# Optimization experiments

Hardware: AMD Instinct MI355X
Metric: run time of the kernel (lower is better)

The kernel has to match this reference:

```python
import jax, jax.numpy as jnp
import numpy as np
from jax import lax

BN_INV = float(1.0 / np.sqrt(1.0 + 1e-5))  # BatchNorm eval: running_mean=0, running_var=1


def _block(x, w, b, g, beta, stride):
    # Conv3x3(stride, pad=1) -> BN(eval) -> ReLU -> MaxPool2
    x = lax.conv_general_dilated(x, w, (stride, stride), [(1, 1), (1, 1)],
                                 dimension_numbers=('NCHW', 'OIHW', 'NCHW'))
    x = x + b[None, :, None, None]
    x = x * (g * BN_INV)[None, :, None, None] + beta[None, :, None, None]
    x = jax.nn.relu(x)
    return lax.reduce_window(x, -jnp.inf, lax.max, (1, 1, 2, 2), (1, 1, 2, 2), 'VALID')


def _gru(x, wi, wh, bi, bh):
    # torch-style GRU, batch_first. x: (B, T, D)
    B = x.shape[0]
    H = wh.shape[1]

    def step(h, xt):
        gi = xt @ wi.T + bi
        gh = h @ wh.T + bh
        ir, iz, inn = jnp.split(gi, 3, axis=1)
        hr, hz, hn = jnp.split(gh, 3, axis=1)
        r = jax.nn.sigmoid(ir + hr)
        z = jax.nn.sigmoid(iz + hz)
        nn_ = jnp.tanh(inn + r * hn)
        h2 = (1.0 - z) * nn_ + z * h
        return h2, h2

    h0 = jnp.zeros((B, H), x.dtype)
    _, ys = lax.scan(step, h0, jnp.swapaxes(x, 0, 1))
    return jnp.swapaxes(ys, 0, 1)  # (B, T, H)


def setup_inputs() -> dict:
    key = jax.random.key(0)
    ks = jax.random.split(key, 32)
    rn = lambda i, shape, s: jax.random.normal(ks[i], shape, jnp.float32) * s
    inp = {
        'support': rn(0, (5, 5, 1, 224, 224), 1.0),
        'query': rn(1, (15, 1, 224, 224), 1.0),
        'conv_w1': rn(2, (32, 1, 3, 3), 0.3), 'conv_b1': rn(3, (32,), 0.1),
        'conv_w2': rn(4, (64, 32, 3, 3), 0.06), 'conv_b2': rn(5, (64,), 0.1),
        'conv_w3': rn(6, (128, 64, 3, 3), 0.04), 'conv_b3': rn(7, (128,), 0.1),
        'conv_w4': rn(8, (256, 128, 3, 3), 0.03), 'conv_b4': rn(9, (256,), 0.1),
        'bn_g1': 1.0 + rn(10, (32,), 0.05), 'bn_be1': rn(11, (32,), 0.05),
        'bn_g2': 1.0 + rn(12, (64,), 0.05), 'bn_be2': rn(13, (64,), 0.05),
        'bn_g3': 1.0 + rn(14, (128,), 0.05), 'bn_be3': rn(15, (128,), 0.05),
        'bn_g4': 1.0 + rn(16, (256,), 0.05), 'bn_be4': rn(17, (256,), 0.05),
        'att_w': rn(18, (64, 256), 0.06), 'att_b': rn(19, (64,), 0.05),
        'gru_wi0': rn(20, (384, 512), 0.04), 'gru_wh0': rn(21, (384, 128), 0.08),
        'gru_bi0': rn(22, (384,), 0.05), 'gru_bh0': rn(23, (384,), 0.05),
        'gru_wi1': rn(24, (384, 128), 0.08), 'gru_wh1': rn(25, (384, 128), 0.08),
        'gru_bi1': rn(26, (384,), 0.05), 'gru_bh1': rn(27, (384,), 0.05),
        'trans_w': rn(28, (1, 128), 0.08), 'trans_b': rn(29, (1,), 0.05),
    }
    return inp


def reference(support, query, conv_w1, conv_b1, conv_w2, conv_b2, conv_w3, conv_b3,
              conv_w4, conv_b4, bn_g1, bn_be1, bn_g2, bn_be2, bn_g3, bn_be3,
              bn_g4, bn_be4, att_w, att_b, gru_wi0, gru_wh0, gru_bi0, gru_bh0,
              gru_wi1, gru_wh1, gru_bi1, gru_bh1, trans_w, trans_b):
    n, k, c, w = support.shape[0], support.shape[1], support.shape[2], support.shape[3]
    qk = query.shape[0]

    def enc(x):
        x = _block(x, conv_w1, conv_b1, bn_g1, bn_be1, 2)
        x = _block(x, conv_w2, conv_b2, bn_g2, bn_be2, 1)
        x = _block(x, conv_w3, conv_b3, bn_g3, bn_be3, 1)
        x = _block(x, conv_w4, conv_b4, bn_g4, bn_be4, 1)
        B, F_, H_, W_ = x.shape
        return x.reshape(B, F_, H_ * W_).transpose(0, 2, 1)  # (B, seq, feat)

    hf = enc(support.reshape(n * k, c, w, w))  # (nk, S, f)
    qf = enc(query)                            # (qk, T, f)

    # ItemQueryAttention: score[q,s,t,u] = sum_h tanh(W(q_t) * W(h_u))
    Wq = qf @ att_w.T + att_b  # (qk, T, h)
    Wh = hf @ att_w.T + att_b  # (nk, S, h)
    scores = jnp.tanh(Wq[:, None, :, None, :] * Wh[None, :, None, :, :]).sum(-1)  # (qk,nk,T,S)
    att = jax.nn.softmax(scores, axis=3)
    attended = jnp.einsum('qsTS,sSf->qsTf', att, hf)  # (qk, nk, T, f)

    T_, f = qf.shape[1], qf.shape[2]
    qrep = jnp.broadcast_to(qf[:, None], (qk, n * k, T_, f))
    x = jnp.concatenate([attended, qrep], axis=-1).reshape(qk * n * k, T_, 2 * f)

    h = _gru(x, gru_wi0, gru_wh0, gru_bi0, gru_bh0)
    h = _gru(h, gru_wi1, gru_wh1, gru_bi1, gru_bh1)

    logits = (h[:, -1, :] @ trans_w.T + trans_b).reshape(qk, n, k).sum(axis=2)  # (qk, n)
    return jax.nn.log_softmax(logits, axis=1)
```

## Files before the change

### kernel.cpp

```cpp
#include <hip/hip_runtime.h>
#include <hip/hip_bf16.h>
#include <math.h>

typedef unsigned short u16;
typedef unsigned int u32;
typedef __attribute__((ext_vector_type(8))) short bf16x8v;
typedef __attribute__((ext_vector_type(4))) float f32x4;

constexpr int NS = 25, NQ = 15, NB = 40;
constexpr int B3 = 375;
constexpr int T49 = 49;
constexpr float BN_INV = 0.9999950000374997f;

constexpr size_t A1_OFF    = 0;
constexpr size_t X2_OFF    = 16056320;
constexpr size_t P2_OFF    = 48168960;
constexpr size_t X3_OFF    = 0;
constexpr size_t P3_OFF    = 56197120;
constexpr size_t X4_OFF    = 16056320;
constexpr size_t FEATT_OFF = 60211200;
constexpr size_t PROJ_OFF  = 24084480;
constexpr size_t ATT_OFF   = 24586240;
constexpr size_t GI_OFF    = 62218240;
constexpr size_t Y0_OFF    = 0;
constexpr size_t HFIN_OFF  = 90442240;
constexpr size_t WBH_OFF   = 91027456;
constexpr size_t WBL_OFF   = 92325888;
constexpr size_t W2_E = 0;
constexpr size_t W3_E = 18432;
constexpr size_t W4_E = 92160;
constexpr size_t AW_E = 387072;
constexpr size_t WI0_E = 403456;
constexpr size_t WI1_E = 600064;

static __device__ __forceinline__ u16 f2b(float f) {
  __hip_bfloat16 h = __float2bfloat16(f);
  return *reinterpret_cast<u16*>(&h);
}
static __device__ __forceinline__ float b2f(u16 u) {
  return __uint_as_float((u32)u << 16);
}
static __device__ __forceinline__ void split8(const float* v, u32* hp, u32* lp) {
  u16 h[8], l[8];
#pragma unroll
  for (int j = 0; j < 8; ++j) {
    const u16 hb = f2b(v[j]);
    h[j] = hb;
    l[j] = f2b(v[j] - b2f(hb));
  }
#pragma unroll
  for (int j = 0; j < 4; ++j) {
    hp[j] = (u32)h[2 * j] | ((u32)h[2 * j + 1] << 16);
    lp[j] = (u32)l[2 * j] | ((u32)l[2 * j + 1] << 16);
  }
}
constexpr float LOG2E = 1.4426950408889634f;
static __device__ __forceinline__ float fsigmoid(float x) {
  return __builtin_amdgcn_rcpf(1.f + __builtin_amdgcn_exp2f(-x * LOG2E));
}
static __device__ __forceinline__ float ftanh(float x) {
  return 1.f - 2.f * __builtin_amdgcn_rcpf(__builtin_amdgcn_exp2f(x * (2.f * LOG2E)) + 1.f);
}

__global__ void cvt_split(const float* __restrict__ x, u16* __restrict__ oh,
                          u16* __restrict__ ol, int n) {
  int i = blockIdx.x * 256 + threadIdx.x;
  if (i >= n) return;
  const float v = x[i];
  const u16 h = f2b(v);
  oh[i] = h;
  ol[i] = f2b(v - b2f(h));
}
__global__ void cvt_conv_w_split(const float* __restrict__ w, u16* __restrict__ oh,
                                 u16* __restrict__ ol, int OC, int IC) {
  const int n = OC * IC * 9;
  int i = blockIdx.x * 256 + threadIdx.x;
  if (i >= n) return;
  const int oc = i / (IC * 9), rem = i % (IC * 9);
  const int e = rem / IC, ic = rem % IC;
  const int ky = e / 3, kx = e % 3;
  const float v = w[((size_t)(oc * IC + ic) * 3 + ky) * 3 + kx];
  const u16 h = f2b(v);
  oh[i] = h;
  ol[i] = f2b(v - b2f(h));
}

__global__ __launch_bounds__(256) void conv1_pool(
    const float* __restrict__ support, const float* __restrict__ query,
    const float* __restrict__ w1, const float* __restrict__ cb1,
    const float* __restrict__ g1, const float* __restrict__ be1,
    float* __restrict__ out) {
  __shared__ float wl[288], scl[32], shl[32], cbl[32];
  const int tid = threadIdx.x;
  for (int l = tid; l < 288; l += 256) wl[l] = w1[l];
  if (tid < 32) { scl[tid] = g1[tid] * BN_INV; shl[tid] = be1[tid]; cbl[tid] = cb1[tid]; }
  __syncthreads();
  const int oc = tid & 31;
  const int p = blockIdx.x * 8 + (tid >> 5);
  const int ox = p % 56, oy = (p / 56) % 56, b = p / 3136;
  const float* in_b = (b < NS) ? (support + (size_t)b * 50176)
                               : (query + (size_t)(b - NS) * 50176);
  const int iy0 = 4 * oy - 1, ix0 = 4 * ox - 1;
  float pat[5][5];
#pragma unroll
  for (int dy = 0; dy < 5; ++dy) {
    const int iy = iy0 + dy;
#pragma unroll
    for (int dx = 0; dx < 5; ++dx) {
      const int ix = ix0 + dx;
      pat[dy][dx] = (iy >= 0 && iy < 224 && ix >= 0 && ix < 224)
                        ? in_b[(size_t)iy * 224 + ix] : 0.f;
    }
  }
  const float* wp = &wl[oc * 9];
  float mx = 0.f;
#pragma unroll
  for (int py = 0; py < 2; ++py)
#pragma unroll
    for (int px = 0; px < 2; ++px) {
      float acc = 0.f;
#pragma unroll
      for (int ky = 0; ky < 3; ++ky)
#pragma unroll
        for (int kx = 0; kx < 3; ++kx)
          acc += pat[2 * py + ky][2 * px + kx] * wp[ky * 3 + kx];
      float v = (acc + cbl[oc]) * scl[oc] + shl[oc];
      mx = fmaxf(mx, v);
    }
  out[(size_t)p * 32 + oc] = mx;
}

__global__ void maxpool2_f32(const float* __restrict__ X, float* __restrict__ Y,
                             int Bn, int H, int W, int C) {
  const int OH = H >> 1, OW = W >> 1;
  const int cpr = C >> 2;
  const int chunks = Bn * OH * OW * cpr;
  for (int i = blockIdx.x * blockDim.x + threadIdx.x; i < chunks;
       i += gridDim.x * blockDim.x) {
    const int c4 = i % cpr, m = i / cpr;
    const int ox = m % OW, oy = (m / OW) % OH, b = m / (OW * OH);
    const size_t base = (((size_t)b * H + 2 * oy) * W + 2 * ox) * C + (c4 << 2);
    const float4 r0 = *(const float4*)&X[base];
    const float4 r1 = *(const float4*)&X[base + C];
    const float4 r2 = *(const float4*)&X[base + (size_t)W * C];
    const float4 r3 = *(const float4*)&X[base + (size_t)W * C + C];
    float4 o;
    o.x = fmaxf(fmaxf(r0.x, r1.x), fmaxf(r2.x, r3.x));
    o.y = fmaxf(fmaxf(r0.y, r1.y), fmaxf(r2.y, r3.y));
    o.z = fmaxf(fmaxf(r0.z, r1.z), fmaxf(r2.z, r3.z));
    o.w = fmaxf(fmaxf(r0.w, r1.w), fmaxf(r2.w, r3.w));
    *(float4*)&Y[(size_t)m * C + (c4 << 2)] = o;
  }
}

template <int AMODE, int EPI>
__global__ __launch_bounds__(256) void sgemm(
    const float* __restrict__ A, const float* __restrict__ A2, int M, int K,
    const u16* __restrict__ Bh, const u16* __restrict__ Bl,
    const float* __restrict__ p0, const float* __restrict__ p1,
    const float* __restrict__ p2, float* __restrict__ Cout, int ldc,
    int H, int W, int IC, int icb) {
  __shared__ u16 Ash[64][72], Asl[64][72];
  __shared__ u16 Bsh[64][72], Bsl[64][72];
  const int tid = threadIdx.x;
  const int lane = tid & 63, wv = tid >> 6;
  const int wy = wv >> 1, wx = wv & 1;
  const int n0 = blockIdx.x * 64, m0 = blockIdx.y * 64;
  f32x4 acc[2][2] = {{{0, 0, 0, 0}, {0, 0, 0, 0}}, {{0, 0, 0, 0}, {0, 0, 0, 0}}};
  for (int k0 = 0; k0 < K; k0 += 64) {
#pragma unroll
    for (int s = 0; s < 2; ++s) {
      const int c = s * 256 + tid;
      const int row = c >> 3, kc = (c & 7) << 3;
      const int gm = m0 + row, gk = k0 + kc;
      float4 x0 = {0, 0, 0, 0}, x1 = {0, 0, 0, 0};
      if (AMODE == 0) {
        if (gm < M && gk < K) {
          const float* p = A + (size_t)gm * K + gk;
          x0 = *(const float4*)p; x1 = *(const float4*)(p + 4);
        }
      } else if (AMODE == 1) {
        if (gm < M) {
          const float* p;
          if (gk < 256) {
            p = A + (size_t)gm * 256 + gk;
          } else {
            const int b = gm / T49, t = gm % T49, q = b / NS;
            p = A2 + (((size_t)(NS + q) * T49 + t) << 8) + (gk - 256);
          }
          x0 = *(const float4*)p; x1 = *(const float4*)(p + 4);
        }
      } else {
        if (gm < M && gk < K) {
          const int ox = gm % W, t_ = gm / W;
          const int oy = t_ % H, b = t_ / H;
          const int e = gk >> icb, ic = gk & (IC - 1);
          const int ky = e / 3, kx = e - 3 * (e / 3);
          const int iy = oy + ky - 1, ix = ox + kx - 1;
          if (iy >= 0 && iy < H && ix >= 0 && ix < W) {
            const float* p = A + (((size_t)b * H + iy) * W + ix) * IC + ic;
            x0 = *(const float4*)p; x1 = *(const float4*)(p + 4);
          }
        }
      }
      float v[8] = {x0.x, x0.y, x0.z, x0.w, x1.x, x1.y, x1.z, x1.w};
      u32 hp[4], lp[4];
      split8(v, hp, lp);
      *(uint4*)&Ash[row][kc] = *(uint4*)hp;
      *(uint4*)&Asl[row][kc] = *(uint4*)lp;
    }
#pragma unroll
    for (int s = 0; s < 2; ++s) {
      const int c = s * 256 + tid;
      const int row = c >> 3, kc = (c & 7) << 3;
      const int gk = k0 + kc;
      uint4 vh = {0u, 0u, 0u, 0u}, vl = {0u, 0u, 0u, 0u};
      if (gk < K) {
        vh = *(const uint4*)&Bh[(size_t)(n0 + row) * K + gk];
        vl = *(const uint4*)&Bl[(size_t)(n0 + row) * K + gk];
      }
      *(uint4*)&Bsh[row][kc] = vh;
      *(uint4*)&Bsl[row][kc] = vl;
    }
    __syncthreads();
#pragma unroll
    for (int kk = 0; kk < 64; kk += 32) {
      const int ko = kk + ((lane >> 4) << 3);
      const int ra0 = wy * 32 + (lane & 15), ra1 = ra0 + 16;
      const int rb0 = wx * 32 + (lane & 15), rb1 = rb0 + 16;
      bf16x8v a0h = *(const bf16x8v*)&Ash[ra0][ko];
      bf16x8v a1h = *(const bf16x8v*)&Ash[ra1][ko];
      bf16x8v b0h = *(const bf16x8v*)&Bsh[rb0][ko];
      bf16x8v b1h = *(const bf16x8v*)&Bsh[rb1][ko];
      bf16x8v a0l = *(const bf16x8v*)&Asl[ra0][ko];
      bf16x8v a1l = *(const bf16x8v*)&Asl[ra1][ko];
      bf16x8v b0l = *(const bf16x8v*)&Bsl[rb0][ko];
      bf16x8v b1l = *(const bf16x8v*)&Bsl[rb1][ko];
      acc[0][0] = __builtin_amdgcn_mfma_f32_16x16x32_bf16(a0h, b0h, acc[0][0], 0, 0, 0);
      acc[0][1] = __builtin_amdgcn_mfma_f32_16x16x32_bf16(a0h, b1h, acc[0][1], 0, 0, 0);
      acc[1][0] = __builtin_amdgcn_mfma_f32_16x16x32_bf16(a1h, b0h, acc[1][0], 0, 0, 0);
      acc[1][1] = __builtin_amdgcn_mfma_f32_16x16x32_bf16(a1h, b1h, acc[1][1], 0, 0, 0);
      acc[0][0] = __builtin_amdgcn_mfma_f32_16x16x32_bf16(a0h, b0l, acc[0][0], 0, 0, 0);
      acc[0][1] = __builtin_amdgcn_mfma_f32_16x16x32_bf16(a0h, b1l, acc[0][1], 0, 0, 0);
      acc[1][0] = __builtin_amdgcn_mfma_f32_16x16x32_bf16(a1h, b0l, acc[1][0], 0, 0, 0);
      acc[1][1] = __builtin_amdgcn_mfma_f32_16x16x32_bf16(a1h, b1l, acc[1][1], 0, 0, 0);
      acc[0][0] = __builtin_amdgcn_mfma_f32_16x16x32_bf16(a0l, b0h, acc[0][0], 0, 0, 0);
      acc[0][1] = __builtin_amdgcn_mfma_f32_16x16x32_bf16(a0l, b1h, acc[0][1], 0, 0, 0);
      acc[1][0] = __builtin_amdgcn_mfma_f32_16x16x32_bf16(a1l, b0h, acc[1][0], 0, 0, 0);
      acc[1][1] = __builtin_amdgcn_mfma_f32_16x16x32_bf16(a1l, b1h, acc[1][1], 0, 0, 0);
    }
    __syncthreads();
  }
#pragma unroll
  for (int r = 0; r < 2; ++r) {
#pragma unroll
    for (int c = 0; c < 2; ++c) {
      const int gn = n0 + wx * 32 + c * 16 + (lane & 15);
      float sc0 = 0.f, sh0 = 0.f;
      if (EPI == 0) { sc0 = p1[gn] * BN_INV; sh0 = p2[gn]; }
#pragma unroll
      for (int i = 0; i < 4; ++i) {
        const int gm = m0 + wy * 32 + r * 16 + ((lane >> 4) << 2) + i;
        if (gm >= M) continue;
        const float a = acc[r][c][i];
        if (EPI == 0) {
          Cout[(size_t)gm * ldc + gn] = fmaxf((a + p0[gn]) * sc0 + sh0, 0.f);
        } else {
          Cout[(size_t)gm * ldc + gn] = a + p0[gn];
        }
      }
    }
  }
}

__global__ __launch_bounds__(256) void attention_f32(
    const float* __restrict__ proj, const float* __restrict__ featT,
    float* __restrict__ attended) {
  __shared__ float WqT[64][9];
  __shared__ float WhT[64][51];
  __shared__ float sc[7][64];
  const int bid = blockIdx.x;
  const int qs = bid / 7, tg = bid - 7 * qs;
  const int q = qs / NS, s = qs - NS * q;
  const int tid = threadIdx.x;
  const float* pq = proj + ((size_t)(NS + q) * T49 + tg * 7) * 64;
  const float* ph = proj + (size_t)s * T49 * 64;
  for (int l = tid; l < 7 * 64; l += 256) WqT[l & 63][l >> 6] = pq[l];
  for (int l = tid; l < T49 * 64; l += 256) WhT[l & 63][l >> 6] = ph[l];
  __syncthreads();
  constexpr float C2LOG2E = 2.8853900817779268f;
  for (int e = tid; e < 343; e += 256) {
    const int tl = e / 49, u = e - 49 * tl;
    float a0 = 0.f, a1 = 0.f, a2 = 0.f, a3 = 0.f;
#pragma unroll
    for (int h = 0; h < 64; h += 4) {
      const float p0 = WqT[h + 0][tl] * WhT[h + 0][u];
      const float p1 = WqT[h + 1][tl] * WhT[h + 1][u];
      const float p2 = WqT[h + 2][tl] * WhT[h + 2][u];
      const float p3 = WqT[h + 3][tl] * WhT[h + 3][u];
      a0 += 1.f - 2.f * __builtin_amdgcn_rcpf(__builtin_amdgcn_exp2f(p0 * C2LOG2E) + 1.f);
      a1 += 1.f - 2.f * __builtin_amdgcn_rcpf(__builtin_amdgcn_exp2f(p1 * C2LOG2E) + 1.f);
      a2 += 1.f - 2.f * __builtin_amdgcn_rcpf(__builtin_amdgcn_exp2f(p2 * C2LOG2E) + 1.f);
      a3 += 1.f - 2.f * __builtin_amdgcn_rcpf(__builtin_amdgcn_exp2f(p3 * C2LOG2E) + 1.f);
    }
    sc[tl][u] = (a0 + a1) + (a2 + a3);
  }
  __syncthreads();
  if (tid < 56) {
    const int t = tid >> 3, g = tid & 7;
    float m = -3.4e38f;
    for (int u = g; u < T49; u += 8) m = fmaxf(m, sc[t][u]);
    m = fmaxf(m, __shfl_xor(m, 4));
    m = fmaxf(m, __shfl_xor(m, 2));
    m = fmaxf(m, __shfl_xor(m, 1));
    float ssum = 0.f;
    for (int u = g; u < T49; u += 8) {
      const float e = __builtin_amdgcn_exp2f((sc[t][u] - m) * LOG2E);
      sc[t][u] = e; ssum += e;
    }
    ssum += __shfl_xor(ssum, 4);
    ssum += __shfl_xor(ssum, 2);
    ssum += __shfl_xor(ssum, 1);
    const float inv = 1.f / ssum;
    for (int u = g; u < T49; u += 8) sc[t][u] *= inv;
  }
  __syncthreads();
  const float* fs = featT + (size_t)s * T49 * 256;
  float* outp = attended + ((size_t)qs * T49 + tg * 7) * 256;
  float acc[7] = {0.f, 0.f, 0.f, 0.f, 0.f, 0.f, 0.f};
  for (int u = 0; u < T49; ++u) {
    const float v = fs[u * 256 + tid];
#pragma unroll
    for (int i = 0; i < 7; ++i) acc[i] += sc[i][u] * v;
  }
#pragma unroll
  for (int i = 0; i < 7; ++i) outp[(size_t)i * 256 + tid] = acc[i];
}

__global__ __launch_bounds__(512) void gru_mfma(
    const float* __restrict__ gi,
    const float* __restrict__ wh,
    const float* __restrict__ bh,
    float* __restrict__ y,
    int store_all) {
  __shared__ u16 hah[2][16][136], hal[2][16][136];
  const int tid = threadIdx.x;
  const int lane = tid & 63, wv = tid >> 6;
  const int r0 = blockIdx.x * 16;
  const int c = lane & 15, rq = lane >> 4;
  const int j = wv * 16 + c;
  const int ko = rq << 3;
  bf16x8v Bhr[3][4], Blr[3][4];
#pragma unroll
  for (int g = 0; g < 3; ++g) {
#pragma unroll
    for (int kk = 0; kk < 4; ++kk) {
      const float* p = wh + (size_t)(g * 128 + j) * 128 + kk * 32 + ko;
      float v[8];
      *(float4*)&v[0] = *(const float4*)p;
      *(float4*)&v[4] = *(const float4*)(p + 4);
      u32 hp[4], lp[4];
      split8(v, hp, lp);
      Bhr[g][kk] = *(bf16x8v*)hp;
      Blr[g][kk] = *(bf16x8v*)lp;
    }
  }
  const float bh0 = bh[j], bh1 = bh[128 + j], bh2 = bh[256 + j];
  int seqs[4];
#pragma unroll
  for (int i = 0; i < 4; ++i) {
    const int s_ = r0 + rq * 4 + i;
    seqs[i] = s_ < B3 ? s_ : B3 - 1;
  }
  for (int i = tid; i < 2 * 16 * 136; i += 512) {
    ((u16*)hah)[i] = 0; ((u16*)hal)[i] = 0;
  }
  float hprev[4] = {0.f, 0.f, 0.f, 0.f};
  __syncthreads();
  float x0[4], x1[4], x2[4];
#pragma unroll
  for (int i = 0; i < 4; ++i) {
    const float* g = gi + (size_t)seqs[i] * T49 * 384 + j;
    x0[i] = g[0]; x1[i] = g[128]; x2[i] = g[256];
  }
  for (int t = 0; t < T49; ++t) {
    const int pr = t & 1, pw = pr ^ 1;
    const int tn = (t + 1 < T49) ? t + 1 : t;
    float y0[4], y1[4], y2[4];
#pragma unroll
    for (int i = 0; i < 4; ++i) {
      const float* g = gi + ((size_t)seqs[i] * T49 + tn) * 384 + j;
      y0[i] = g[0]; y1[i] = g[128]; y2[i] = g[256];
    }
    bf16x8v Ah[4], Al[4];
#pragma unroll
    for (int kk = 0; kk < 4; ++kk) {
      Ah[kk] = *(const bf16x8v*)&hah[pr][c][kk * 32 + ko];
      Al[kk] = *(const bf16x8v*)&hal[pr][c][kk * 32 + ko];
    }
    f32x4 aR = {0, 0, 0, 0}, aZ = {0, 0, 0, 0}, aN = {0, 0, 0, 0};
#pragma unroll
    for (int kk = 0; kk < 4; ++kk) {
      aR = __builtin_amdgcn_mfma_f32_16x16x32_bf16(Ah[kk], Bhr[0][kk], aR, 0, 0, 0);
      aZ = __builtin_amdgcn_mfma_f32_16x16x32_bf16(Ah[kk], Bhr[1][kk], aZ, 0, 0, 0);
      aN = __builtin_amdgcn_mfma_f32_16x16x32_bf16(Ah[kk], Bhr[2][kk], aN, 0, 0, 0);
    }
#pragma unroll
    for (int kk = 0; kk < 4; ++kk) {
      aR = __builtin_amdgcn_mfma_f32_16x16x32_bf16(Ah[kk], Blr[0][kk], aR, 0, 0, 0);
      aZ = __builtin_amdgcn_mfma_f32_16x16x32_bf16(Ah[kk], Blr[1][kk], aZ, 0, 0, 0);
      aN = __builtin_amdgcn_mfma_f32_16x16x32_bf16(Ah[kk], Blr[2][kk], aN, 0, 0, 0);
    }
#pragma unroll
    for (int kk = 0; kk < 4; ++kk) {
      aR = __builtin_amdgcn_mfma_f32_16x16x32_bf16(Al[kk], Bhr[0][kk], aR, 0, 0, 0);
      aZ = __builtin_amdgcn_mfma_f32_16x16x32_bf16(Al[kk], Bhr[1][kk], aZ, 0, 0, 0);
      aN = __builtin_amdgcn_mfma_f32_16x16x32_bf16(Al[kk], Bhr[2][kk], aN, 0, 0, 0);
    }
#pragma unroll
    for (int i = 0; i < 4; ++i) {
      const int row = rq * 4 + i;
      const float r_ = fsigmoid(x0[i] + aR[i] + bh0);
      const float z_ = fsigmoid(x1[i] + aZ[i] + bh1);
      const float n_ = ftanh(x2[i] + r_ * (aN[i] + bh2));
      const float hn = (1.f - z_) * n_ + z_ * hprev[i];
      hprev[i] = hn;
      const u16 hb = f2b(hn);
      hah[pw][row][j] = hb;
      hal[pw][row][j] = f2b(hn - b2f(hb));
      const int seq = r0 + row;
      if (seq < B3) {
        if (store_all) y[((size_t)seq * T49 + t) * 128 + j] = hn;
        else if (t == T49 - 1) y[(size_t)seq * 128 + j] = hn;
      }
    }
    __syncthreads();
#pragma unroll
    for (int i = 0; i < 4; ++i) { x0[i] = y0[i]; x1[i] = y1[i]; x2[i] = y2[i]; }
  }
}

__global__ __launch_bounds__(512) void head_kernel(
    const float* __restrict__ hf, const float* __restrict__ tw,
    const float* __restrict__ tb, float* __restrict__ out) {
  __shared__ float lg[B3];
  const int tid = threadIdx.x;
  if (tid < B3) {
    const float* h = hf + (size_t)tid * 128;
    float acc = tb[0];
    for (int k = 0; k < 128; ++k) acc += h[k] * tw[k];
    lg[tid] = acc;
  }
  __syncthreads();
  if (tid < NQ) {
    float cls[5];
#pragma unroll
    for (int n = 0; n < 5; ++n) {
      float s = 0.f;
#pragma unroll
      for (int k = 0; k < 5; ++k) s += lg[tid * 25 + n * 5 + k];
      cls[n] = s;
    }
    float m = cls[0];
#pragma unroll
    for (int n = 1; n < 5; ++n) m = fmaxf(m, cls[n]);
    float se = 0.f;
#pragma unroll
    for (int n = 0; n < 5; ++n) se += expf(cls[n] - m);
    const float lse = m + logf(se);
#pragma unroll
    for (int n = 0; n < 5; ++n) out[tid * 5 + n] = cls[n] - lse;
  }
}

extern "C" void kernel_launch(void* const* d_in, const int* in_sizes, int n_in,
                              void* d_out, int out_size, void* d_ws,
                              size_t ws_size, hipStream_t stream) {
  (void)in_sizes; (void)n_in; (void)out_size; (void)ws_size;
  const float* support = (const float*)d_in[0];
  const float* query   = (const float*)d_in[1];
  const float* cw1 = (const float*)d_in[2];  const float* cb1 = (const float*)d_in[3];
  const float* cw2 = (const float*)d_in[4];  const float* cb2 = (const float*)d_in[5];
  const float* cw3 = (const float*)d_in[6];  const float* cb3 = (const float*)d_in[7];
  const float* cw4 = (const float*)d_in[8];  const float* cb4 = (const float*)d_in[9];
  const float* g1  = (const float*)d_in[10]; const float* be1 = (const float*)d_in[11];
  const float* g2  = (const float*)d_in[12]; const float* be2 = (const float*)d_in[13];
  const float* g3  = (const float*)d_in[14]; const float* be3 = (const float*)d_in[15];
  const float* g4  = (const float*)d_in[16]; const float* be4 = (const float*)d_in[17];
  const float* aw  = (const float*)d_in[18]; const float* ab  = (const float*)d_in[19];
  const float* wi0 = (const float*)d_in[20]; const float* wh0 = (const float*)d_in[21];
  const float* bi0 = (const float*)d_in[22]; const float* bh0 = (const float*)d_in[23];
  const float* wi1 = (const float*)d_in[24]; const float* wh1 = (const float*)d_in[25];
  const float* bi1 = (const float*)d_in[26]; const float* bh1 = (const float*)d_in[27];
  const float* tw  = (const float*)d_in[28]; const float* tb  = (const float*)d_in[29];

  char* ws = (char*)d_ws;
  float* out = (float*)d_out;
  float* A1    = (float*)(ws + A1_OFF);
  float* X2    = (float*)(ws + X2_OFF);
  float* P2    = (float*)(ws + P2_OFF);
  float* X3    = (float*)(ws + X3_OFF);
  float* P3    = (float*)(ws + P3_OFF);
  float* X4    = (float*)(ws + X4_OFF);
  float* FEATT = (float*)(ws + FEATT_OFF);
  float* PROJ  = (float*)(ws + PROJ_OFF);
  float* ATT   = (float*)(ws + ATT_OFF);
  float* GI    = (float*)(ws + GI_OFF);
  float* Y0    = (float*)(ws + Y0_OFF);
  float* HFIN  = (float*)(ws + HFIN_OFF);
  u16* WBH = (u16*)(ws + WBH_OFF);
  u16* WBL = (u16*)(ws + WBL_OFF);

  cvt_conv_w_split<<<(64 * 288 + 255) / 256, 256, 0, stream>>>(cw2, WBH + W2_E, WBL + W2_E, 64, 32);
  cvt_conv_w_split<<<(128 * 576 + 255) / 256, 256, 0, stream>>>(cw3, WBH + W3_E, WBL + W3_E, 128, 64);
  cvt_conv_w_split<<<(256 * 1152 + 255) / 256, 256, 0, stream>>>(cw4, WBH + W4_E, WBL + W4_E, 256, 128);
  cvt_split<<<(64 * 256 + 255) / 256, 256, 0, stream>>>(aw, WBH + AW_E, WBL + AW_E, 64 * 256);
  cvt_split<<<(384 * 512 + 255) / 256, 256, 0, stream>>>(wi0, WBH + WI0_E, WBL + WI0_E, 384 * 512);
  cvt_split<<<(384 * 128 + 255) / 256, 256, 0, stream>>>(wi1, WBH + WI1_E, WBL + WI1_E, 384 * 128);

  conv1_pool<<<15680, 256, 0, stream>>>(support, query, cw1, cb1, g1, be1, A1);
  sgemm<2, 0><<<dim3(1, 1960), 256, 0, stream>>>(
      A1, nullptr, 125440, 288, WBH + W2_E, WBL + W2_E, cb2, g2, be2, X2, 64,
      56, 56, 32, 5);
  maxpool2_f32<<<1960, 256, 0, stream>>>(X2, P2, NB, 56, 56, 64);
  sgemm<2, 0><<<dim3(2, 490), 256, 0, stream>>>(
      P2, nullptr, 31360, 576, WBH + W3_E, WBL + W3_E, cb3, g3, be3, X3, 128,
      28, 28, 64, 6);
  maxpool2_f32<<<980, 256, 0, stream>>>(X3, P3, NB, 28, 28, 128);
  sgemm<2, 0><<<dim3(4, 123), 256, 0, stream>>>(
      P3, nullptr, 7840, 1152, WBH + W4_E, WBL + W4_E, cb4, g4, be4, X4, 256,
      14, 14, 128, 7);
  maxpool2_f32<<<490, 256, 0, stream>>>(X4, FEATT, NB, 14, 14, 256);

  sgemm<0, 1><<<dim3(1, 31), 256, 0, stream>>>(
      FEATT, nullptr, NB * T49, 256, WBH + AW_E, WBL + AW_E, ab, nullptr,
      nullptr, PROJ, 64, 0, 0, 0, 0);
  attention_f32<<<B3 * 7, 256, 0, stream>>>(PROJ, FEATT, ATT);

  sgemm<1, 1><<<dim3(6, 288), 256, 0, stream>>>(
      ATT, FEATT, B3 * T49, 512, WBH + WI0_E, WBL + WI0_E, bi0, nullptr,
      nullptr, GI, 384, 0, 0, 0, 0);
  gru_mfma<<<24, 512, 0, stream>>>(GI, wh0, bh0, Y0, 1);
  sgemm<0, 1><<<dim3(6, 288), 256, 0, stream>>>(
      Y0, nullptr, B3 * T49, 128, WBH + WI1_E, WBL + WI1_E, bi1, nullptr,
      nullptr, GI, 384, 0, 0, 0, 0);
  gru_mfma<<<24, 512, 0, stream>>>(GI, wh1, bh1, HFIN, 0);

  head_kernel<<<1, 512, 0, stream>>>(HFIN, tw, tb, out);
}
```

Measured before the change: 409.5 us.

## Replace MFMA GRU recurrence with fp32 VALU kernel, two sequences per block

The recurrent GRU kernel changes from 24 blocks of 16 sequences each, which used split-bf16 MFMA with three products per step, to 188 blocks of 768 threads that each handle 2 sequences. Each thread holds one full fp32 row of the hidden-weight matrix in registers and computes a 128-long dot product against the hidden state in LDS. This spreads the serial 49-step recurrence over many more CUs and drops the bf16 hi/lo split. In exchange it uses heavy register pressure (128 floats of weights per thread), does more scalar FMA work per sequence, and needs two barriers per step.

```diff
diff --git a/kernel.cpp b/kernel.cpp
--- a/kernel.cpp
+++ b/kernel.cpp
@@ -60,6 +60,12 @@
 }
 static __device__ __forceinline__ float ftanh(float x) {
   return 1.f - 2.f * __builtin_amdgcn_rcpf(__builtin_amdgcn_exp2f(x * (2.f * LOG2E)) + 1.f);
+}
+static __device__ __forceinline__ void barrier_lgkm() {
+  __builtin_amdgcn_sched_barrier(0);
+  asm volatile("s_waitcnt lgkmcnt(0)" ::: "memory");
+  __builtin_amdgcn_s_barrier();
+  __builtin_amdgcn_sched_barrier(0);
 }
 
 __global__ void cvt_split(const float* __restrict__ x, u16* __restrict__ oh,
@@ -337,106 +343,61 @@
   for (int i = 0; i < 7; ++i) outp[(size_t)i * 256 + tid] = acc[i];
 }
 
-__global__ __launch_bounds__(512) void gru_mfma(
+constexpr int GSEQ = 2;
+__global__ __launch_bounds__(768) void gru_valu(
     const float* __restrict__ gi,
     const float* __restrict__ wh,
     const float* __restrict__ bh,
     float* __restrict__ y,
     int store_all) {
-  __shared__ u16 hah[2][16][136], hal[2][16][136];
+  __shared__ float hl[GSEQ][128];
+  __shared__ float ghl[GSEQ][384];
+  __shared__ float gil[GSEQ][384];
   const int tid = threadIdx.x;
-  const int lane = tid & 63, wv = tid >> 6;
-  const int r0 = blockIdx.x * 16;
-  const int c = lane & 15, rq = lane >> 4;
-  const int j = wv * 16 + c;
-  const int ko = rq << 3;
-  bf16x8v Bhr[3][4], Blr[3][4];
-#pragma unroll
-  for (int g = 0; g < 3; ++g) {
-#pragma unroll
-    for (int kk = 0; kk < 4; ++kk) {
-      const float* p = wh + (size_t)(g * 128 + j) * 128 + kk * 32 + ko;
-      float v[8];
-      *(float4*)&v[0] = *(const float4*)p;
-      *(float4*)&v[4] = *(const float4*)(p + 4);
-      u32 hp[4], lp[4];
-      split8(v, hp, lp);
-      Bhr[g][kk] = *(bf16x8v*)hp;
-      Blr[g][kk] = *(bf16x8v*)lp;
-    }
-  }
-  const float bh0 = bh[j], bh1 = bh[128 + j], bh2 = bh[256 + j];
-  int seqs[4];
-#pragma unroll
-  for (int i = 0; i < 4; ++i) {
-    const int s_ = r0 + rq * 4 + i;
-    seqs[i] = s_ < B3 ? s_ : B3 - 1;
-  }
-  for (int i = tid; i < 2 * 16 * 136; i += 512) {
-    ((u16*)hah)[i] = 0; ((u16*)hal)[i] = 0;
-  }
-  float hprev[4] = {0.f, 0.f, 0.f, 0.f};
+  const int ss = tid >= 384 ? 1 : 0;
+  const int n = tid - 384 * ss;
+  const int r0 = blockIdx.x * GSEQ;
+  int seq = r0 + ss; if (seq >= B3) seq = B3 - 1;
+  const bool wr = (r0 + ss) < B3;
+  float4 w4[32];
+#pragma unroll
+  for (int c = 0; c < 32; ++c) w4[c] = *(const float4*)&wh[(size_t)n * 128 + c * 4];
+  const float bhn = bh[n];
+  for (int i = tid; i < GSEQ * 128; i += 768) hl[i >> 7][i & 127] = 0.f;
+  const float* gseq = gi + (size_t)seq * T49 * 384;
+  float xc = gseq[n];
   __syncthreads();
-  float x0[4], x1[4], x2[4];
-#pragma unroll
-  for (int i = 0; i < 4; ++i) {
-    const float* g = gi + (size_t)seqs[i] * T49 * 384 + j;
-    x0[i] = g[0]; x1[i] = g[128]; x2[i] = g[256];
-  }
   for (int t = 0; t < T49; ++t) {
-    const int pr = t & 1, pw = pr ^ 1;
+    gil[ss][n] = xc;
     const int tn = (t + 1 < T49) ? t + 1 : t;
-    float y0[4], y1[4], y2[4];
-#pragma unroll
-    for (int i = 0; i < 4; ++i) {
-      const float* g = gi + ((size_t)seqs[i] * T49 + tn) * 384 + j;
-      y0[i] = g[0]; y1[i] = g[128]; y2[i] = g[256];
-    }
-    bf16x8v Ah[4], Al[4];
-#pragma unroll
-    for (int kk = 0; kk < 4; ++kk) {
-      Ah[kk] = *(const bf16x8v*)&hah[pr][c][kk * 32 + ko];
-      Al[kk] = *(const bf16x8v*)&hal[pr][c][kk * 32 + ko];
-    }
-    f32x4 aR = {0, 0, 0, 0}, aZ = {0, 0, 0, 0}, aN = {0, 0, 0, 0};
-#pragma unroll
-    for (int kk = 0; kk < 4; ++kk) {
-      aR = __builtin_amdgcn_mfma_f32_16x16x32_bf16(Ah[kk], Bhr[0][kk], aR, 0, 0, 0);
-      aZ = __builtin_amdgcn_mfma_f32_16x16x32_bf16(Ah[kk], Bhr[1][kk], aZ, 0, 0, 0);
-      aN = __builtin_amdgcn_mfma_f32_16x16x32_bf16(Ah[kk], Bhr[2][kk], aN, 0, 0, 0);
-    }
-#pragma unroll
-    for (int kk = 0; kk < 4; ++kk) {
-      aR = __builtin_amdgcn_mfma_f32_16x16x32_bf16(Ah[kk], Blr[0][kk], aR, 0, 0, 0);
-      aZ = __builtin_amdgcn_mfma_f32_16x16x32_bf16(Ah[kk], Blr[1][kk], aZ, 0, 0, 0);
-      aN = __builtin_amdgcn_mfma_f32_16x16x32_bf16(Ah[kk], Blr[2][kk], aN, 0, 0, 0);
-    }
-#pragma unroll
-    for (int kk = 0; kk < 4; ++kk) {
-      aR = __builtin_amdgcn_mfma_f32_16x16x32_bf16(Al[kk], Bhr[0][kk], aR, 0, 0, 0);
-      aZ = __builtin_amdgcn_mfma_f32_16x16x32_bf16(Al[kk], Bhr[1][kk], aZ, 0, 0, 0);
-      aN = __builtin_amdgcn_mfma_f32_16x16x32_bf16(Al[kk], Bhr[2][kk], aN, 0, 0, 0);
-    }
-#pragma unroll
-    for (int i = 0; i < 4; ++i) {
-      const int row = rq * 4 + i;
-      const float r_ = fsigmoid(x0[i] + aR[i] + bh0);
-      const float z_ = fsigmoid(x1[i] + aZ[i] + bh1);
-      const float n_ = ftanh(x2[i] + r_ * (aN[i] + bh2));
-      const float hn = (1.f - z_) * n_ + z_ * hprev[i];
-      hprev[i] = hn;
-      const u16 hb = f2b(hn);
-      hah[pw][row][j] = hb;
-      hal[pw][row][j] = f2b(hn - b2f(hb));
-      const int seq = r0 + row;
-      if (seq < B3) {
-        if (store_all) y[((size_t)seq * T49 + t) * 128 + j] = hn;
-        else if (t == T49 - 1) y[(size_t)seq * 128 + j] = hn;
+    const float xnext = gseq[(size_t)tn * 384 + n];
+    float a0 = 0.f, a1 = 0.f, a2 = 0.f, a3 = 0.f;
+#pragma unroll
+    for (int c = 0; c < 32; c += 4) {
+      const float4 h0 = *(const float4*)&hl[ss][(c + 0) * 4];
+      const float4 h1 = *(const float4*)&hl[ss][(c + 1) * 4];
+      const float4 h2 = *(const float4*)&hl[ss][(c + 2) * 4];
+      const float4 h3 = *(const float4*)&hl[ss][(c + 3) * 4];
+      a0 += (h0.x * w4[c + 0].x + h0.y * w4[c + 0].y) + (h0.z * w4[c + 0].z + h0.w * w4[c + 0].w);
+      a1 += (h1.x * w4[c + 1].x + h1.y * w4[c + 1].y) + (h1.z * w4[c + 1].z + h1.w * w4[c + 1].w);
+      a2 += (h2.x * w4[c + 2].x + h2.y * w4[c + 2].y) + (h2.z * w4[c + 2].z + h2.w * w4[c + 2].w);
+      a3 += (h3.x * w4[c + 3].x + h3.y * w4[c + 3].y) + (h3.z * w4[c + 3].z + h3.w * w4[c + 3].w);
+    }
+    ghl[ss][n] = ((a0 + a1) + (a2 + a3)) + bhn;
+    barrier_lgkm();
+    if (n < 128) {
+      const float r_ = fsigmoid(gil[ss][n] + ghl[ss][n]);
+      const float z_ = fsigmoid(gil[ss][128 + n] + ghl[ss][128 + n]);
+      const float n_ = ftanh(gil[ss][256 + n] + r_ * ghl[ss][256 + n]);
+      const float hn2 = (1.f - z_) * n_ + z_ * hl[ss][n];
+      hl[ss][n] = hn2;
+      if (wr) {
+        if (store_all) y[((size_t)(r0 + ss) * T49 + t) * 128 + n] = hn2;
+        else if (t == T49 - 1) y[(size_t)(r0 + ss) * 128 + n] = hn2;
       }
     }
-    __syncthreads();
-#pragma unroll
-    for (int i = 0; i < 4; ++i) { x0[i] = y0[i]; x1[i] = y1[i]; x2[i] = y2[i]; }
+    barrier_lgkm();
+    xc = xnext;
   }
 }
 
@@ -540,11 +501,11 @@
   sgemm<1, 1><<<dim3(6, 288), 256, 0, stream>>>(
       ATT, FEATT, B3 * T49, 512, WBH + WI0_E, WBL + WI0_E, bi0, nullptr,
       nullptr, GI, 384, 0, 0, 0, 0);
-  gru_mfma<<<24, 512, 0, stream>>>(GI, wh0, bh0, Y0, 1);
+  gru_valu<<<188, 768, 0, stream>>>(GI, wh0, bh0, Y0, 1);
   sgemm<0, 1><<<dim3(6, 288), 256, 0, stream>>>(
       Y0, nullptr, B3 * T49, 128, WBH + WI1_E, WBL + WI1_E, bi1, nullptr,
       nullptr, GI, 384, 0, 0, 0, 0);
-  gru_mfma<<<24, 512, 0, stream>>>(GI, wh1, bh1, HFIN, 0);
+  gru_valu<<<188, 768, 0, stream>>>(GI, wh1, bh1, HFIN, 0);
 
   head_kernel<<<1, 512, 0, stream>>>(HFIN, tw, tb, out);
 }
```

New measurement: 465.8 us. 13.7% more time.
